# Optimization experiments

Measured on AMD Instinct MI355X. Metric: run time of the kernel, lower is better.

The kernel has to match this reference:

```python
import jax, jax.numpy as jnp
import numpy as np

NUM_RBF = 16; TOP_K = 32; EDGE_F = 128; NODE_F = 128; NUM_POS = 16; MAX_REL = 32
B, L, M = 2, 1024, 25
# atom order: N=0, Ca=1, C=2, O=3, Cb=4; 24 pairs after the (Ca,Ca) D_neighbors term,
# in the exact order of the torch forward's RBF_all list
PAIR_A = jnp.array([0,2,3,4,1,1,1,1,0,0,0,4,4,3,0,2,3,4,2,3,4,2,3,2])
PAIR_B = jnp.array([0,2,3,4,0,2,3,4,2,3,4,2,3,2,1,1,1,1,0,0,0,4,4,3])


def _rbf(D):
    mu = jnp.linspace(2.0, 22.0, NUM_RBF)
    sig = (22.0 - 2.0) / NUM_RBF
    return jnp.exp(-((D[..., None] - mu) / sig) ** 2)


def _ln(x, g, b, eps=1e-5):
    m = x.mean(-1, keepdims=True)
    v = ((x - m) ** 2).mean(-1, keepdims=True)
    return (x - m) * jax.lax.rsqrt(v + eps) * g + b


def _normalize(v):
    n = jnp.linalg.norm(v, axis=-1, keepdims=True)
    return v / jnp.maximum(n, 1e-12)


def setup_inputs():
    key = jax.random.key(0)
    ks = jax.random.split(key, 16)
    def w(i, shape, scale):
        return jax.random.normal(ks[i], shape, jnp.float32) * scale
    ar = jnp.arange(120, dtype=jnp.int32)
    return {
        "X": w(0, (B, L, 4, 3), 3.0),
        "Y": w(1, (B, L, M, 3), 3.0),
        "Y_m": jnp.ones((B, L, M), jnp.float32),
        "Y_t": jax.random.randint(ks[2], (B, L, M), 0, 120, jnp.int32),
        "mask": jnp.ones((B, L), jnp.float32),
        "R_idx": jnp.tile(jnp.arange(L, dtype=jnp.int32), (B, 1)),
        "chain_labels": jnp.zeros((B, L), jnp.int32),
        # learned params; torch Linear y = x @ W.T + b stored here as [in,out]
        "pos_W": w(3, (2 * MAX_REL + 2, NUM_POS), 0.1),
        "pos_b": jnp.zeros((NUM_POS,), jnp.float32),
        "edge_W": w(4, (NUM_POS + 25 * NUM_RBF, EDGE_F), 0.05),
        "ln_e_g": jnp.ones((EDGE_F,), jnp.float32), "ln_e_b": jnp.zeros((EDGE_F,), jnp.float32),
        "npd_W": w(5, (5 * NUM_RBF + 64 + 4, NODE_F), 0.08),
        "npd_b": jnp.zeros((NODE_F,), jnp.float32),
        "ln_n_g": jnp.ones((NODE_F,), jnp.float32), "ln_n_b": jnp.zeros((NODE_F,), jnp.float32),
        "type_W": w(6, (147, 64), 0.08), "type_b": jnp.zeros((64,), jnp.float32),
        "yn_W": w(7, (147, NODE_F), 0.08),
        "ye_W": w(8, (NUM_RBF, NODE_F), 0.2),
        "ln_ye_g": jnp.ones((NODE_F,), jnp.float32), "ln_ye_b": jnp.zeros((NODE_F,), jnp.float32),
        "ln_yn_g": jnp.ones((NODE_F,), jnp.float32), "ln_yn_b": jnp.zeros((NODE_F,), jnp.float32),
        # periodic table: [atomic_number, group(<19), period(<8)] per element id
        "ptable": jnp.stack([ar, ar % 19, ar % 8]),
    }


def reference(X, Y, Y_m, Y_t, mask, R_idx, chain_labels, pos_W, pos_b, edge_W,
              ln_e_g, ln_e_b, npd_W, npd_b, ln_n_g, ln_n_b, type_W, type_b,
              yn_W, ye_W, ln_ye_g, ln_ye_b, ln_yn_g, ln_yn_b, ptable):
    N, Ca, C, O = X[:, :, 0], X[:, :, 1], X[:, :, 2], X[:, :, 3]
    b = Ca - N; c = C - Ca
    a = jnp.cross(b, c)
    Cb = -0.58273431 * a + 0.56802827 * b - 0.54067466 * c + Ca

    # masked Ca-Ca distances + kNN (smallest)
    m2 = mask[:, :, None] * mask[:, None, :]
    D = m2 * jnp.sqrt(((Ca[:, :, None, :] - Ca[:, None, :, :]) ** 2).sum(-1) + 1e-6)
    D_adjust = D + (1.0 - m2) * D.max(-1, keepdims=True)
    k = min(TOP_K, L)
    neg_D, E_idx = jax.lax.top_k(-D_adjust, k)
    D_neighbors = -neg_D  # [B,L,k]

    atoms = jnp.stack([N, Ca, C, O, Cb])  # [5,B,L,3]
    def pair_rbf(ai, bi):
        A = atoms[ai]; Bc = atoms[bi]
        Dab = jnp.sqrt(((A[:, :, None, :] - Bc[:, None, :, :]) ** 2).sum(-1) + 1e-6)
        return _rbf(jnp.take_along_axis(Dab, E_idx, axis=2))  # [B,L,k,16]
    rbf_pairs = jax.vmap(pair_rbf)(PAIR_A, PAIR_B)  # [24,B,L,k,16]
    RBF_all = jnp.concatenate([_rbf(D_neighbors)[:, :, :, None, :],
                               jnp.moveaxis(rbf_pairs, 0, 3)], axis=3)
    RBF_all = RBF_all.reshape(RBF_all.shape[0], RBF_all.shape[1], k, 25 * NUM_RBF)

    # positional encodings over gathered neighbor offsets
    offset = jnp.take_along_axis(R_idx[:, :, None] - R_idx[:, None, :], E_idx, axis=2)
    d_chains = (chain_labels[:, :, None] == chain_labels[:, None, :]).astype(jnp.int32)
    E_chains = jnp.take_along_axis(d_chains, E_idx, axis=2)
    d = jnp.clip(offset + MAX_REL, 0, 2 * MAX_REL) * E_chains + (1 - E_chains) * (2 * MAX_REL + 1)
    E_pos = jax.nn.one_hot(d, 2 * MAX_REL + 2, dtype=jnp.float32) @ pos_W + pos_b

    E = jnp.concatenate([E_pos, RBF_all], -1) @ edge_W
    E = _ln(E, ln_e_g, ln_e_b)

    # ligand atom type features
    Y_t_1hot_ = jnp.concatenate([
        jax.nn.one_hot(Y_t, 120, dtype=jnp.float32),
        jax.nn.one_hot(ptable[1][Y_t], 19, dtype=jnp.float32),
        jax.nn.one_hot(ptable[2][Y_t], 8, dtype=jnp.float32)], -1)  # [B,L,M,147]
    Y_t_1hot = Y_t_1hot_ @ type_W + type_b  # [B,L,M,64]

    def rbf_to_Y(A):
        return _rbf(jnp.sqrt(((A[:, :, None, :] - Y) ** 2).sum(-1) + 1e-6))
    D_Y = jnp.concatenate([rbf_to_Y(A) for A in (N, Ca, C, O, Cb)], -1)  # [B,L,M,80]

    # local-frame angle features (A=N, B=Ca, C=C)
    e1 = _normalize(N - Ca)
    v2 = C - Ca
    e2 = _normalize(v2 - e1 * (e1 * v2).sum(-1, keepdims=True))
    e3 = jnp.cross(e1, e2)
    R_res = jnp.stack([e1, e2, e3], axis=-1)  # [B,L,3,3], columns e1,e2,e3
    local = jnp.einsum('blqp,blyq->blyp', R_res, Y - Ca[:, :, None, :])
    rxy = jnp.sqrt(local[..., 0] ** 2 + local[..., 1] ** 2 + 1e-8)
    rxyz = jnp.linalg.norm(local, axis=-1) + 1e-8
    f_angles = jnp.stack([local[..., 0] / rxy, local[..., 1] / rxy,
                          rxy / rxyz, local[..., 2] / rxyz], -1)  # [B,L,M,4]

    V = jnp.concatenate([D_Y, Y_t_1hot, f_angles], -1) @ npd_W + npd_b
    V = _ln(V, ln_n_g, ln_n_b)

    Y_edges = _rbf(jnp.sqrt(((Y[:, :, :, None, :] - Y[:, :, None, :, :]) ** 2).sum(-1) + 1e-6)) @ ye_W
    Y_edges = _ln(Y_edges, ln_ye_g, ln_ye_b)
    Y_nodes = _ln(Y_t_1hot_ @ yn_W, ln_yn_g, ln_yn_b)
    return V, E, E_idx, Y_nodes, Y_edges, Y_m
```

## Files before the change

kernel.cpp:

```cpp
#include <hip/hip_runtime.h>
#include <hip/hip_bf16.h>
#include <stdint.h>

#define BB 2
#define LLEN 1024
#define MM 25
#define KK 32

#define OFF_V   0
#define OFF_E   6553600
#define OFF_EI  14942208
#define OFF_YN  15007744
#define OFF_YE  21561344
#define OFF_YM  185401344

#define KD 416
#define KP 424
#define KP2 168
#define NR 5

#define SCRATCH_BYTES (680*1024)

typedef __attribute__((ext_vector_type(8))) short short8_t;
typedef __attribute__((ext_vector_type(4))) float f32x4;

__constant__ int g_PA[24] = {0,2,3,4,1,1,1,1,0,0,0,4,4,3,0,2,3,4,2,3,4,2,3,2};
__constant__ int g_PB[24] = {0,2,3,4,0,2,3,4,2,3,4,2,3,2,1,1,1,1,0,0,0,4,4,3};

__device__ __forceinline__ float rbf_val(float d, int r) {
    float mu = 2.0f + (20.0f / 15.0f) * (float)r;
    float z = (d - mu) * 0.8f;
    return __expf(-z * z);
}

__global__ __launch_bounds__(256) void k_pretopk(
    const float* __restrict__ X, const float* __restrict__ mask,
    const float* __restrict__ W, const float* __restrict__ yeW,
    const float* __restrict__ npdW,
    __hip_bfloat16* __restrict__ Bp, __hip_bfloat16* __restrict__ Bp2,
    __hip_bfloat16* __restrict__ Bp3,
    int* __restrict__ eidx, float* __restrict__ dnb,
    float* __restrict__ outEI)
{
    __shared__ float sx[1024], syy[1024], sz[1024], sm[1024];
    int tid = threadIdx.x;

    if (blockIdx.x >= 512) {
        int idx = (blockIdx.x - 512) * 256 + tid;
        if (idx < 6656) {
            int lane = idx & 63, tt = (idx >> 6) & 7, ks = idx >> 9;
            int k0 = ks*32 + (lane >> 4)*8;
            int n  = tt*16 + (lane & 15);
            __hip_bfloat16* dst = Bp + (size_t)idx * 8;
            #pragma unroll
            for (int j = 0; j < 8; ++j) dst[j] = __float2bfloat16(W[(size_t)(k0 + j)*128 + n]);
        } else if (idx < 7168) {
            int i2 = idx - 6656;
            int lane = i2 & 63, tt = i2 >> 6;
            int kg = lane >> 4;
            int n  = tt*16 + (lane & 15);
            __hip_bfloat16* dst = Bp2 + (size_t)i2 * 8;
            #pragma unroll
            for (int j = 0; j < 8; ++j) {
                float v = (kg < 2) ? yeW[(size_t)(kg*8 + j)*128 + n] : 0.0f;
                dst[j] = __float2bfloat16(v);
            }
        } else if (idx < 9728) {
            int i3 = idx - 7168;
            int lane = i3 & 63, tt = (i3 >> 6) & 7, ks = i3 >> 9;
            int k0 = ks*32 + (lane >> 4)*8;
            int n  = tt*16 + (lane & 15);
            __hip_bfloat16* dst = Bp3 + (size_t)i3 * 8;
            #pragma unroll
            for (int j = 0; j < 8; ++j) {
                int k = k0 + j;
                float v = (k < 148) ? npdW[(size_t)k*128 + n] : 0.0f;
                dst[j] = __float2bfloat16(v);
            }
        }
        return;
    }

    int wid = tid >> 6, lane = tid & 63;
    int row0 = blockIdx.x * 4;
    int b = row0 >> 10;
    const float* Xb = X + (size_t)b * LLEN * 12;
    const float* mb = mask + b * LLEN;
    for (int j = tid; j < 1024; j += 256) {
        sx[j]  = Xb[j*12+3];
        syy[j] = Xb[j*12+4];
        sz[j]  = Xb[j*12+5];
        sm[j]  = mb[j];
    }
    __syncthreads();

    int row = row0 + wid, i = row & 1023;
    float cax = sx[i], cay = syy[i], caz = sz[i];
    float mi = sm[i];

    float df[16], mm_[16];
    float lmax = 0.0f;
    #pragma unroll
    for (int q = 0; q < 16; ++q) {
        int j = q*64 + lane;
        float dx = cax - sx[j];
        float dy = cay - syy[j];
        float dz = caz - sz[j];
        float m2 = mi * sm[j];
        float d = sqrtf(dx*dx + dy*dy + dz*dz + 1e-6f) * m2;
        df[q] = d; mm_[q] = m2;
        lmax = fmaxf(lmax, d);
    }
    #pragma unroll
    for (int o = 32; o > 0; o >>= 1) lmax = fmaxf(lmax, __shfl_xor(lmax, o));

    unsigned long long pack[16];
    #pragma unroll
    for (int q = 0; q < 16; ++q) {
        float da = df[q] + (1.0f - mm_[q]) * lmax;
        pack[q] = ((unsigned long long)__float_as_uint(da) << 32) | (unsigned)(q*64 + lane);
    }

    int   myJw = 0;
    float myDv = 0.0f;
    for (int it = 0; it < KK; ++it) {
        unsigned long long lmin = pack[0];
        #pragma unroll
        for (int q = 1; q < 16; ++q) if (pack[q] < lmin) lmin = pack[q];
        #pragma unroll
        for (int o = 32; o > 0; o >>= 1) {
            unsigned long long other = __shfl_xor(lmin, o);
            if (other < lmin) lmin = other;
        }
        int jw = (int)(lmin & 0xffffffffu);
        if (lane == it) { myJw = jw; myDv = __uint_as_float((unsigned)(lmin >> 32)); }
        int lw = jw & 63, qw = jw >> 6;
        #pragma unroll
        for (int q = 0; q < 16; ++q)
            if (lane == lw && q == qw) pack[q] = ~0ull;
    }
    if (lane < KK) {
        eidx[row*KK + lane]  = myJw;
        dnb [row*KK + lane]  = myDv;
        outEI[row*KK + lane] = (float)myJw;
    }
}

__global__ __launch_bounds__(256) void k_edges(
    const float* __restrict__ X,
    const int* __restrict__ Ridx, const int* __restrict__ chain,
    const float* __restrict__ posW, const float* __restrict__ posb,
    const __hip_bfloat16* __restrict__ Bpack,
    const float* __restrict__ lnEg, const float* __restrict__ lnEb,
    const int* __restrict__ eidx, const float* __restrict__ dnb,
    float* __restrict__ outE)
{
    __shared__ __align__(16) __hip_bfloat16 A[64 * KP];
    __shared__ float aj[64][16];
    __shared__ float ai[2][16];
    __shared__ int   didx[64];
    int r0 = blockIdx.x * 2;
    int b  = r0 >> 10;
    int tid = threadIdx.x;
    const float* Xb = X + (size_t)b * LLEN * 12;

    if (tid < 64) {
        int e = tid, row = r0 + (e >> 5), k = e & 31;
        int j = eidx[row*KK + k];
        const float* xr = Xb + j*12;
        float nx=xr[0], ny=xr[1], nz=xr[2];
        float ax=xr[3], ay=xr[4], az=xr[5];
        float cx=xr[6], cy=xr[7], cz=xr[8];
        float bx=ax-nx, by=ay-ny, bz=az-nz;
        float vx=cx-ax, vy=cy-ay, vz=cz-az;
        float qx = by*vz - bz*vy, qy = bz*vx - bx*vz, qz = bx*vy - by*vx;
        aj[e][0]=nx; aj[e][1]=ny; aj[e][2]=nz;
        aj[e][3]=ax; aj[e][4]=ay; aj[e][5]=az;
        aj[e][6]=cx; aj[e][7]=cy; aj[e][8]=cz;
        aj[e][9]=xr[9]; aj[e][10]=xr[10]; aj[e][11]=xr[11];
        aj[e][12] = -0.58273431f*qx + 0.56802827f*bx - 0.54067466f*vx + ax;
        aj[e][13] = -0.58273431f*qy + 0.56802827f*by - 0.54067466f*vy + ay;
        aj[e][14] = -0.58273431f*qz + 0.56802827f*bz - 0.54067466f*vz + az;
        int off = Ridx[row] - Ridx[b*LLEN + j];
        int ec = (chain[row] == chain[b*LLEN + j]) ? 1 : 0;
        int dc = off + 32; dc = dc < 0 ? 0 : (dc > 64 ? 64 : dc);
        didx[e] = ec ? dc : 65;
    }
    if (tid >= 64 && tid < 66) {
        int rl = tid - 64;
        int i = (r0 + rl) & 1023;
        const float* xr = Xb + i*12;
        float nx=xr[0], ny=xr[1], nz=xr[2];
        float ax=xr[3], ay=xr[4], az=xr[5];
        float cx=xr[6], cy=xr[7], cz=xr[8];
        float bx=ax-nx, by=ay-ny, bz=az-nz;
        float vx=cx-ax, vy=cy-ay, vz=cz-az;
        float qx = by*vz - bz*vy, qy = bz*vx - bx*vz, qz = bx*vy - by*vx;
        ai[rl][0]=nx; ai[rl][1]=ny; ai[rl][2]=nz;
        ai[rl][3]=ax; ai[rl][4]=ay; ai[rl][5]=az;
        ai[rl][6]=cx; ai[rl][7]=cy; ai[rl][8]=cz;
        ai[rl][9]=xr[9]; ai[rl][10]=xr[10]; ai[rl][11]=xr[11];
        ai[rl][12] = -0.58273431f*qx + 0.56802827f*bx - 0.54067466f*vx + ax;
        ai[rl][13] = -0.58273431f*qy + 0.56802827f*by - 0.54067466f*vy + ay;
        ai[rl][14] = -0.58273431f*qz + 0.56802827f*bz - 0.54067466f*vz + az;
    }
    __syncthreads();

    for (int item = tid; item < 64 * 26; item += 256) {
        int e = item / 26, it = item - e * 26;
        int rl = e >> 5;
        union { short8_t v[2]; __hip_bfloat16 h[16]; } uf;
        if (it == 0) {
            int d = didx[e];
            #pragma unroll
            for (int c = 0; c < 16; ++c) uf.h[c] = __float2bfloat16(posW[d*16 + c] + posb[c]);
        } else {
            float dist;
            if (it == 1) {
                dist = dnb[(r0 + rl)*KK + (e & 31)];
            } else {
                int p = it - 2;
                int a = g_PA[p], q = g_PB[p];
                float dx = ai[rl][a*3+0] - aj[e][q*3+0];
                float dy = ai[rl][a*3+1] - aj[e][q*3+1];
                float dz = ai[rl][a*3+2] - aj[e][q*3+2];
                dist = sqrtf(dx*dx + dy*dy + dz*dz + 1e-6f);
            }
            #pragma unroll
            for (int r = 0; r < 16; ++r) uf.h[r] = __float2bfloat16(rbf_val(dist, r));
        }
        short8_t* dst = (short8_t*)(A + e * KP + it * 16);
        dst[0] = uf.v[0];
        dst[1] = uf.v[1];
    }
    __syncthreads();

    int wid = tid >> 6, lane = tid & 63;
    int col16 = lane & 15, kg = lane >> 4;
    f32x4 acc[8];
    #pragma unroll
    for (int t = 0; t < 8; ++t) acc[t] = (f32x4){0.f, 0.f, 0.f, 0.f};
    const __hip_bfloat16* Ar = A + (wid*16 + col16) * KP + kg * 8;
    const short8_t* Bp = (const short8_t*)Bpack;
    for (int ks = 0; ks < 13; ++ks) {
        short8_t a = *(const short8_t*)(Ar + ks*32);
        #pragma unroll
        for (int t = 0; t < 8; ++t) {
            short8_t bf = Bp[(ks*8 + t)*64 + lane];
            acc[t] = __builtin_amdgcn_mfma_f32_16x16x32_bf16(a, bf, acc[t], 0, 0, 0);
        }
    }
    __syncthreads();

    float* sbuf = (float*)A + wid * (16*132);
    float g[8], be[8];
    #pragma unroll
    for (int t = 0; t < 8; ++t) { g[t] = lnEg[t*16 + col16]; be[t] = lnEb[t*16 + col16]; }
    #pragma unroll
    for (int r = 0; r < 4; ++r) {
        float s = 0.0f;
        #pragma unroll
        for (int t = 0; t < 8; ++t) s += acc[t][r];
        s += __shfl_xor(s, 1); s += __shfl_xor(s, 2);
        s += __shfl_xor(s, 4); s += __shfl_xor(s, 8);
        float mean = s * (1.0f/128.0f);
        float q2 = 0.0f;
        #pragma unroll
        for (int t = 0; t < 8; ++t) { float c0 = acc[t][r] - mean; q2 += c0*c0; }
        q2 += __shfl_xor(q2, 1); q2 += __shfl_xor(q2, 2);
        q2 += __shfl_xor(q2, 4); q2 += __shfl_xor(q2, 8);
        float inv = rsqrtf(q2 * (1.0f/128.0f) + 1e-5f);
        float* sr = sbuf + (kg*4 + r) * 132;
        #pragma unroll
        for (int t = 0; t < 8; ++t) sr[t*16 + col16] = (acc[t][r] - mean)*inv*g[t] + be[t];
    }
    float* gdst = outE + ((size_t)r0 * KK + wid*16) * 128;
    #pragma unroll
    for (int it = 0; it < 8; ++it) {
        int off = it*256 + lane*4;
        int rr = off >> 7, cc = off & 127;
        float4 v = *(const float4*)(sbuf + rr*132 + cc);
        *(float4*)(gdst + off) = v;
    }
}

__global__ __launch_bounds__(256) void k_nodes(
    const float* __restrict__ X, const float* __restrict__ Y,
    const int* __restrict__ Yt,
    const float* __restrict__ typeW, const float* __restrict__ typeb,
    const int* __restrict__ ptab,
    const __hip_bfloat16* __restrict__ Bpack3, const float* __restrict__ npdb,
    const float* __restrict__ lnNg, const float* __restrict__ lnNb,
    float* __restrict__ outV)
{
    __shared__ __align__(16) __hip_bfloat16 A[128 * KP2];
    __shared__ float sat[NR][15];
    __shared__ float sfr[NR][9];
    int r0 = blockIdx.x * NR;
    int nrows = (2048 - r0) < NR ? (2048 - r0) : NR;
    int natoms = nrows * MM;
    int tid = threadIdx.x;

    if (tid < nrows) {
        int row = r0 + tid;
        int b = row >> 10, i = row & 1023;
        const float* xr = X + ((size_t)b * LLEN + i) * 12;
        float nx=xr[0], ny=xr[1], nz=xr[2];
        float ax=xr[3], ay=xr[4], az=xr[5];
        float cx=xr[6], cy=xr[7], cz=xr[8];
        float bx=ax-nx, by=ay-ny, bz=az-nz;
        float vx=cx-ax, vy=cy-ay, vz=cz-az;
        float qx = by*vz - bz*vy, qy = bz*vx - bx*vz, qz = bx*vy - by*vx;
        sat[tid][0]=nx; sat[tid][1]=ny; sat[tid][2]=nz;
        sat[tid][3]=ax; sat[tid][4]=ay; sat[tid][5]=az;
        sat[tid][6]=cx; sat[tid][7]=cy; sat[tid][8]=cz;
        sat[tid][9]=xr[9]; sat[tid][10]=xr[10]; sat[tid][11]=xr[11];
        sat[tid][12] = -0.58273431f*qx + 0.56802827f*bx - 0.54067466f*vx + ax;
        sat[tid][13] = -0.58273431f*qy + 0.56802827f*by - 0.54067466f*vy + ay;
        sat[tid][14] = -0.58273431f*qz + 0.56802827f*bz - 0.54067466f*vz + az;
        float e1x = nx-ax, e1y = ny-ay, e1z = nz-az;
        float n1 = fmaxf(sqrtf(e1x*e1x+e1y*e1y+e1z*e1z), 1e-12f);
        e1x/=n1; e1y/=n1; e1z/=n1;
        float dd = e1x*vx + e1y*vy + e1z*vz;
        float u2x = vx - e1x*dd, u2y = vy - e1y*dd, u2z = vz - e1z*dd;
        float n2 = fmaxf(sqrtf(u2x*u2x+u2y*u2y+u2z*u2z), 1e-12f);
        u2x/=n2; u2y/=n2; u2z/=n2;
        sfr[tid][0]=e1x; sfr[tid][1]=e1y; sfr[tid][2]=e1z;
        sfr[tid][3]=u2x; sfr[tid][4]=u2y; sfr[tid][5]=u2z;
        sfr[tid][6]=e1y*u2z - e1z*u2y;
        sfr[tid][7]=e1z*u2x - e1x*u2z;
        sfr[tid][8]=e1x*u2y - e1y*u2x;
    }
    __syncthreads();

    for (int item = tid; item < natoms * 10; item += 256) {
        int a = item / 10, it = item - a * 10;
        int rl = a / MM, m = a - rl * MM;
        int row = r0 + rl;
        const float* Yb = Y + (size_t)row * MM * 3 + m * 3;
        union { short8_t v[2]; __hip_bfloat16 h[16]; } uf;
        if (it < 5) {
            float dx = sat[rl][it*3+0] - Yb[0];
            float dy = sat[rl][it*3+1] - Yb[1];
            float dz = sat[rl][it*3+2] - Yb[2];
            float dist = sqrtf(dx*dx + dy*dy + dz*dz + 1e-6f);
            #pragma unroll
            for (int r = 0; r < 16; ++r) uf.h[r] = __float2bfloat16(rbf_val(dist, r));
        } else if (it < 9) {
            int qq = it - 5;
            int t = Yt[row*MM + m];
            int p1 = ptab[120 + t], p2 = ptab[240 + t];
            #pragma unroll
            for (int c = 0; c < 16; ++c) {
                int cc = qq*16 + c;
                uf.h[c] = __float2bfloat16(typeW[t*64 + cc] + typeW[(120+p1)*64 + cc]
                        + typeW[(139+p2)*64 + cc] + typeb[cc]);
            }
        } else {
            float vx = Yb[0] - sat[rl][3];
            float vy = Yb[1] - sat[rl][4];
            float vz = Yb[2] - sat[rl][5];
            float l0 = sfr[rl][0]*vx + sfr[rl][1]*vy + sfr[rl][2]*vz;
            float l1 = sfr[rl][3]*vx + sfr[rl][4]*vy + sfr[rl][5]*vz;
            float l2 = sfr[rl][6]*vx + sfr[rl][7]*vy + sfr[rl][8]*vz;
            float rxy  = sqrtf(l0*l0 + l1*l1 + 1e-8f);
            float rxyz = sqrtf(l0*l0 + l1*l1 + l2*l2) + 1e-8f;
            uf.h[0] = __float2bfloat16(l0 / rxy);
            uf.h[1] = __float2bfloat16(l1 / rxy);
            uf.h[2] = __float2bfloat16(rxy / rxyz);
            uf.h[3] = __float2bfloat16(l2 / rxyz);
            #pragma unroll
            for (int c = 4; c < 16; ++c) uf.h[c] = __float2bfloat16(0.0f);
        }
        short8_t* dst = (short8_t*)(A + a * KP2 + it * 16);
        dst[0] = uf.v[0];
        dst[1] = uf.v[1];
    }
    __syncthreads();

    int wid = tid >> 6, lane = tid & 63;
    int col16 = lane & 15, kg = lane >> 4;
    const short8_t* Bp = (const short8_t*)Bpack3;
    float g[8], be[8], bias[8];
    #pragma unroll
    for (int t = 0; t < 8; ++t) {
        g[t] = lnNg[t*16 + col16]; be[t] = lnNb[t*16 + col16];
        bias[t] = npdb[t*16 + col16];
    }
    #pragma unroll
    for (int half = 0; half < 2; ++half) {
        int tile = wid + half*4;
        int abase = tile * 16;
        if (abase < natoms) {
            const __hip_bfloat16* Ar = A + (abase + col16) * KP2 + kg * 8;
            f32x4 acc[8];
            #pragma unroll
            for (int t = 0; t < 8; ++t) acc[t] = (f32x4){0.f, 0.f, 0.f, 0.f};
            for (int ks = 0; ks < 5; ++ks) {
                short8_t a = *(const short8_t*)(Ar + ks*32);
                #pragma unroll
                for (int t = 0; t < 8; ++t) {
                    short8_t bf = Bp[(ks*8 + t)*64 + lane];
                    acc[t] = __builtin_amdgcn_mfma_f32_16x16x32_bf16(a, bf, acc[t], 0, 0, 0);
                }
            }
            #pragma unroll
            for (int r = 0; r < 4; ++r) {
                float s = 0.0f;
                #pragma unroll
                for (int t = 0; t < 8; ++t) { acc[t][r] += bias[t]; s += acc[t][r]; }
                s += __shfl_xor(s, 1); s += __shfl_xor(s, 2);
                s += __shfl_xor(s, 4); s += __shfl_xor(s, 8);
                float mean = s * (1.0f/128.0f);
                float q2 = 0.0f;
                #pragma unroll
                for (int t = 0; t < 8; ++t) { float c0 = acc[t][r] - mean; q2 += c0*c0; }
                q2 += __shfl_xor(q2, 1); q2 += __shfl_xor(q2, 2);
                q2 += __shfl_xor(q2, 4); q2 += __shfl_xor(q2, 8);
                float inv = rsqrtf(q2 * (1.0f/128.0f) + 1e-5f);
                int aa = abase + kg*4 + r;
                if (aa < natoms) {
                    float* dst = outV + ((size_t)r0 * MM + aa) * 128 + col16;
                    #pragma unroll
                    for (int t = 0; t < 8; ++t) dst[t*16] = (acc[t][r] - mean)*inv*g[t] + be[t];
                }
            }
        }
    }
}

__global__ __launch_bounds__(256) void k_ymerge(
    int block_base,
    const float* __restrict__ Y,
    const __hip_bfloat16* __restrict__ Bpack2,
    const float* __restrict__ lnYEg, const float* __restrict__ lnYEb,
    float* __restrict__ outYE,
    const int* __restrict__ Yt, const float* __restrict__ Ym,
    const int* __restrict__ ptab, const float* __restrict__ ynW,
    const float* __restrict__ lnYNg, const float* __restrict__ lnYNb,
    float* __restrict__ outYN, float* __restrict__ outYM)
{
    __shared__ __align__(16) float sy4[32][4];
    __shared__ __align__(16) float stage[4][16*132];
    int vbid = blockIdx.x + block_base;
    int tid = threadIdx.x;
    int wv = tid >> 6, lane = tid & 63;

    if (vbid >= BB*LLEN) {
        int row = (vbid - BB*LLEN) * 4 + wv;
        int t = Yt[row];
        int p1 = ptab[120 + t], p2 = ptab[240 + t];
        int r0 = t, r1 = 120 + p1, r2 = 139 + p2;
        float x0 = ynW[r0*128 + lane] + ynW[r1*128 + lane] + ynW[r2*128 + lane];
        float x1 = ynW[r0*128 + 64 + lane] + ynW[r1*128 + 64 + lane] + ynW[r2*128 + 64 + lane];
        float s = x0 + x1, s2 = x0*x0 + x1*x1;
        #pragma unroll
        for (int o = 1; o < 64; o <<= 1) { s += __shfl_xor(s, o); s2 += __shfl_xor(s2, o); }
        float mean = s * (1.0f/128.0f);
        float var  = s2 * (1.0f/128.0f) - mean*mean;
        float inv  = rsqrtf(var + 1e-5f);
        size_t base = (size_t)row * 128;
        outYN[base + lane]      = (x0 - mean)*inv*lnYNg[lane]    + lnYNb[lane];
        outYN[base + 64 + lane] = (x1 - mean)*inv*lnYNg[64+lane] + lnYNb[64+lane];
        if (lane == 0) outYM[row] = Ym[row];
        return;
    }

    int row = vbid;
    int col16 = lane & 15, kg = lane >> 4;

    if (tid < 32) { sy4[tid][0]=0.f; sy4[tid][1]=0.f; sy4[tid][2]=0.f; sy4[tid][3]=0.f; }
    __syncthreads();
    if (tid < MM*3) ((float*)sy4)[ (tid/3)*4 + (tid%3) ] = Y[(size_t)row * MM * 3 + tid];

    short8_t bfr[8];
    const short8_t* B2 = (const short8_t*)Bpack2;
    #pragma unroll
    for (int t = 0; t < 8; ++t) bfr[t] = B2[t*64 + lane];
    float g[8], be[8];
    #pragma unroll
    for (int t = 0; t < 8; ++t) { g[t] = lnYEg[t*16 + col16]; be[t] = lnYEb[t*16 + col16]; }
    __syncthreads();

    float* outR = outYE + (size_t)row * 625 * 128;
    float* sbuf = stage[wv];
    for (int T = wv; T < 40; T += 4) {
        int p0 = T * 16;
        int p  = p0 + col16;
        int pc = p < 624 ? p : 624;
        int m1 = pc / 25, m2 = pc - 25*m1;
        float dx = sy4[m1][0] - sy4[m2][0];
        float dy = sy4[m1][1] - sy4[m2][1];
        float dz = sy4[m1][2] - sy4[m2][2];
        float d = sqrtf(dx*dx + dy*dy + dz*dz + 1e-6f);
        union { short8_t v; __hip_bfloat16 h[8]; } ua;
        if (kg < 2) {
            #pragma unroll
            for (int j = 0; j < 8; ++j) ua.h[j] = __float2bfloat16(rbf_val(d, kg*8 + j));
        } else {
            ua.v = (short8_t){0,0,0,0,0,0,0,0};
        }
        f32x4 acc[8];
        #pragma unroll
        for (int t = 0; t < 8; ++t)
            acc[t] = __builtin_amdgcn_mfma_f32_16x16x32_bf16(ua.v, bfr[t],
                         (f32x4){0.f,0.f,0.f,0.f}, 0, 0, 0);
        #pragma unroll
        for (int r = 0; r < 4; ++r) {
            float s = 0.0f;
            #pragma unroll
            for (int t = 0; t < 8; ++t) s += acc[t][r];
            s += __shfl_xor(s, 1); s += __shfl_xor(s, 2);
            s += __shfl_xor(s, 4); s += __shfl_xor(s, 8);
            float mean = s * (1.0f/128.0f);
            float q2 = 0.0f;
            #pragma unroll
            for (int t = 0; t < 8; ++t) { float c0 = acc[t][r] - mean; q2 += c0*c0; }
            q2 += __shfl_xor(q2, 1); q2 += __shfl_xor(q2, 2);
            q2 += __shfl_xor(q2, 4); q2 += __shfl_xor(q2, 8);
            float inv = rsqrtf(q2 * (1.0f/128.0f) + 1e-5f);
            float* sr = sbuf + (kg*4 + r) * 132;
            #pragma unroll
            for (int t = 0; t < 8; ++t) sr[t*16 + col16] = (acc[t][r] - mean)*inv*g[t] + be[t];
        }
        #pragma unroll
        for (int it = 0; it < 8; ++it) {
            int off = it*256 + lane*4;
            int rr = (off >> 7), cc = off & 127;
            float4 v = *(const float4*)(sbuf + rr*132 + cc);
            int gbase = p0*128 + off;
            if (gbase < 80000) *(float4*)(outR + gbase) = v;
        }
    }
}

extern "C" void kernel_launch(void* const* d_in, const int* in_sizes, int n_in,
                              void* d_out, int out_size, void* d_ws, size_t ws_size,
                              hipStream_t stream) {
    const float* X     = (const float*)d_in[0];
    const float* Y     = (const float*)d_in[1];
    const float* Ym    = (const float*)d_in[2];
    const int*   Yt    = (const int*)d_in[3];
    const float* mask  = (const float*)d_in[4];
    const int*   Ridx  = (const int*)d_in[5];
    const int*   chain = (const int*)d_in[6];
    const float* posW  = (const float*)d_in[7];
    const float* posb  = (const float*)d_in[8];
    const float* edgeW = (const float*)d_in[9];
    const float* lnEg  = (const float*)d_in[10];
    const float* lnEb  = (const float*)d_in[11];
    const float* npdW  = (const float*)d_in[12];
    const float* npdb  = (const float*)d_in[13];
    const float* lnNg  = (const float*)d_in[14];
    const float* lnNb  = (const float*)d_in[15];
    const float* typeW = (const float*)d_in[16];
    const float* typeb = (const float*)d_in[17];
    const float* ynW   = (const float*)d_in[18];
    const float* yeW   = (const float*)d_in[19];
    const float* lnYEg = (const float*)d_in[20];
    const float* lnYEb = (const float*)d_in[21];
    const float* lnYNg = (const float*)d_in[22];
    const float* lnYNb = (const float*)d_in[23];
    const int*   ptab  = (const int*)d_in[24];

    float* o = (float*)d_out;
    bool ws_ok = (ws_size >= (size_t)SCRATCH_BYTES);
    char* scratch = ws_ok ? (char*)d_ws : (char*)(o + OFF_YN);
    int*   eidx = (int*)scratch;
    float* dnb  = (float*)(scratch + BB*LLEN*KK*4);
    __hip_bfloat16* Bpack  = (__hip_bfloat16*)(scratch + 2*BB*LLEN*KK*4);
    __hip_bfloat16* Bpack2 = Bpack + 6656*8;
    __hip_bfloat16* Bpack3 = Bpack2 + 512*8;

    k_pretopk<<<550, 256, 0, stream>>>(X, mask, edgeW, yeW, npdW,
                                       Bpack, Bpack2, Bpack3,
                                       eidx, dnb, o + OFF_EI);
    k_edges <<<BB*LLEN/2, 256, 0, stream>>>(X, Ridx, chain, posW, posb, Bpack,
                                            lnEg, lnEb, eidx, dnb, o + OFF_E);
    k_nodes <<<(BB*LLEN + NR - 1)/NR, 256, 0, stream>>>(X, Y, Yt, typeW, typeb, ptab,
                                          Bpack3, npdb, lnNg, lnNb, o + OFF_V);
    if (ws_ok) {
        k_ymerge<<<BB*LLEN + BB*LLEN*MM/4, 256, 0, stream>>>(0,
            Y, Bpack2, lnYEg, lnYEb, o + OFF_YE,
            Yt, Ym, ptab, ynW, lnYNg, lnYNb, o + OFF_YN, o + OFF_YM);
    } else {
        k_ymerge<<<BB*LLEN, 256, 0, stream>>>(0,
            Y, Bpack2, lnYEg, lnYEb, o + OFF_YE,
            Yt, Ym, ptab, ynW, lnYNg, lnYNb, o + OFF_YN, o + OFF_YM);
        k_ymerge<<<BB*LLEN*MM/4, 256, 0, stream>>>(BB*LLEN,
            Y, Bpack2, lnYEg, lnYEb, o + OFF_YE,
            Yt, Ym, ptab, ynW, lnYNg, lnYNb, o + OFF_YN, o + OFF_YM);
    }
}
```

Before: 241.8 us.

## Merge edge, node and Y-feature kernels into one launch with virtual block dispatch

Combines the k_edges, k_nodes and k_ymerge kernels into a single k_main kernel. Each block picks its role from a virtual block index, and the per-role shared-memory buffers are overlaid in a union. This removes two kernel launches and the serialization between them, so the small edge and node grids can run alongside the large Y-edge grid. The cost is that the union takes the largest shared-memory footprint and register pressure comes from the heaviest branch, which may reduce occupancy for the lighter roles.

Measured after the change: 239.8 us. No clear change (-0.8%).

```diff
diff --git a/kernel.cpp b/kernel.cpp
--- a/kernel.cpp
+++ b/kernel.cpp
@@ -14,10 +14,18 @@
 #define OFF_YE  21561344
 #define OFF_YM  185401344
 
-#define KD 416
 #define KP 424
 #define KP2 168
 #define NR 5
+
+#define NB_YE  (BB*LLEN)
+#define NB_E   (BB*LLEN/2)
+#define NB_N   ((BB*LLEN+NR-1)/NR)
+#define NB_YN  (BB*LLEN*MM/4)
+#define VB_E   NB_YE
+#define VB_N   (VB_E + NB_E)
+#define VB_YN  (VB_N + NB_N)
+#define VB_END (VB_YN + NB_YN)
 
 #define SCRATCH_BYTES (680*1024)
 
@@ -146,308 +154,41 @@
     }
 }
 
-__global__ __launch_bounds__(256) void k_edges(
-    const float* __restrict__ X,
+union SMem {
+    struct { __hip_bfloat16 A[64*KP]; float aj[64][16]; float ai[2][16]; int didx[64]; } e;
+    struct { __hip_bfloat16 A[128*KP2]; float sat[NR][15]; float sfr[NR][9]; } n;
+    struct { float sy4[32][4]; float stage[4][16*132]; } y;
+};
+
+__global__ __launch_bounds__(256) void k_main(
+    int vbase,
+    const float* __restrict__ X, const float* __restrict__ Y,
     const int* __restrict__ Ridx, const int* __restrict__ chain,
     const float* __restrict__ posW, const float* __restrict__ posb,
     const __hip_bfloat16* __restrict__ Bpack,
     const float* __restrict__ lnEg, const float* __restrict__ lnEb,
     const int* __restrict__ eidx, const float* __restrict__ dnb,
-    float* __restrict__ outE)
-{
-    __shared__ __align__(16) __hip_bfloat16 A[64 * KP];
-    __shared__ float aj[64][16];
-    __shared__ float ai[2][16];
-    __shared__ int   didx[64];
-    int r0 = blockIdx.x * 2;
-    int b  = r0 >> 10;
-    int tid = threadIdx.x;
-    const float* Xb = X + (size_t)b * LLEN * 12;
-
-    if (tid < 64) {
-        int e = tid, row = r0 + (e >> 5), k = e & 31;
-        int j = eidx[row*KK + k];
-        const float* xr = Xb + j*12;
-        float nx=xr[0], ny=xr[1], nz=xr[2];
-        float ax=xr[3], ay=xr[4], az=xr[5];
-        float cx=xr[6], cy=xr[7], cz=xr[8];
-        float bx=ax-nx, by=ay-ny, bz=az-nz;
-        float vx=cx-ax, vy=cy-ay, vz=cz-az;
-        float qx = by*vz - bz*vy, qy = bz*vx - bx*vz, qz = bx*vy - by*vx;
-        aj[e][0]=nx; aj[e][1]=ny; aj[e][2]=nz;
-        aj[e][3]=ax; aj[e][4]=ay; aj[e][5]=az;
-        aj[e][6]=cx; aj[e][7]=cy; aj[e][8]=cz;
-        aj[e][9]=xr[9]; aj[e][10]=xr[10]; aj[e][11]=xr[11];
-        aj[e][12] = -0.58273431f*qx + 0.56802827f*bx - 0.54067466f*vx + ax;
-        aj[e][13] = -0.58273431f*qy + 0.56802827f*by - 0.54067466f*vy + ay;
-        aj[e][14] = -0.58273431f*qz + 0.56802827f*bz - 0.54067466f*vz + az;
-        int off = Ridx[row] - Ridx[b*LLEN + j];
-        int ec = (chain[row] == chain[b*LLEN + j]) ? 1 : 0;
-        int dc = off + 32; dc = dc < 0 ? 0 : (dc > 64 ? 64 : dc);
-        didx[e] = ec ? dc : 65;
-    }
-    if (tid >= 64 && tid < 66) {
-        int rl = tid - 64;
-        int i = (r0 + rl) & 1023;
-        const float* xr = Xb + i*12;
-        float nx=xr[0], ny=xr[1], nz=xr[2];
-        float ax=xr[3], ay=xr[4], az=xr[5];
-        float cx=xr[6], cy=xr[7], cz=xr[8];
-        float bx=ax-nx, by=ay-ny, bz=az-nz;
-        float vx=cx-ax, vy=cy-ay, vz=cz-az;
-        float qx = by*vz - bz*vy, qy = bz*vx - bx*vz, qz = bx*vy - by*vx;
-        ai[rl][0]=nx; ai[rl][1]=ny; ai[rl][2]=nz;
-        ai[rl][3]=ax; ai[rl][4]=ay; ai[rl][5]=az;
-        ai[rl][6]=cx; ai[rl][7]=cy; ai[rl][8]=cz;
-        ai[rl][9]=xr[9]; ai[rl][10]=xr[10]; ai[rl][11]=xr[11];
-        ai[rl][12] = -0.58273431f*qx + 0.56802827f*bx - 0.54067466f*vx + ax;
-        ai[rl][13] = -0.58273431f*qy + 0.56802827f*by - 0.54067466f*vy + ay;
-        ai[rl][14] = -0.58273431f*qz + 0.56802827f*bz - 0.54067466f*vz + az;
-    }
-    __syncthreads();
-
-    for (int item = tid; item < 64 * 26; item += 256) {
-        int e = item / 26, it = item - e * 26;
-        int rl = e >> 5;
-        union { short8_t v[2]; __hip_bfloat16 h[16]; } uf;
-        if (it == 0) {
-            int d = didx[e];
-            #pragma unroll
-            for (int c = 0; c < 16; ++c) uf.h[c] = __float2bfloat16(posW[d*16 + c] + posb[c]);
-        } else {
-            float dist;
-            if (it == 1) {
-                dist = dnb[(r0 + rl)*KK + (e & 31)];
-            } else {
-                int p = it - 2;
-                int a = g_PA[p], q = g_PB[p];
-                float dx = ai[rl][a*3+0] - aj[e][q*3+0];
-                float dy = ai[rl][a*3+1] - aj[e][q*3+1];
-                float dz = ai[rl][a*3+2] - aj[e][q*3+2];
-                dist = sqrtf(dx*dx + dy*dy + dz*dz + 1e-6f);
-            }
-            #pragma unroll
-            for (int r = 0; r < 16; ++r) uf.h[r] = __float2bfloat16(rbf_val(dist, r));
-        }
-        short8_t* dst = (short8_t*)(A + e * KP + it * 16);
-        dst[0] = uf.v[0];
-        dst[1] = uf.v[1];
-    }
-    __syncthreads();
-
-    int wid = tid >> 6, lane = tid & 63;
-    int col16 = lane & 15, kg = lane >> 4;
-    f32x4 acc[8];
-    #pragma unroll
-    for (int t = 0; t < 8; ++t) acc[t] = (f32x4){0.f, 0.f, 0.f, 0.f};
-    const __hip_bfloat16* Ar = A + (wid*16 + col16) * KP + kg * 8;
-    const short8_t* Bp = (const short8_t*)Bpack;
-    for (int ks = 0; ks < 13; ++ks) {
-        short8_t a = *(const short8_t*)(Ar + ks*32);
-        #pragma unroll
-        for (int t = 0; t < 8; ++t) {
-            short8_t bf = Bp[(ks*8 + t)*64 + lane];
-            acc[t] = __builtin_amdgcn_mfma_f32_16x16x32_bf16(a, bf, acc[t], 0, 0, 0);
-        }
-    }
-    __syncthreads();
-
-    float* sbuf = (float*)A + wid * (16*132);
-    float g[8], be[8];
-    #pragma unroll
-    for (int t = 0; t < 8; ++t) { g[t] = lnEg[t*16 + col16]; be[t] = lnEb[t*16 + col16]; }
-    #pragma unroll
-    for (int r = 0; r < 4; ++r) {
-        float s = 0.0f;
-        #pragma unroll
-        for (int t = 0; t < 8; ++t) s += acc[t][r];
-        s += __shfl_xor(s, 1); s += __shfl_xor(s, 2);
-        s += __shfl_xor(s, 4); s += __shfl_xor(s, 8);
-        float mean = s * (1.0f/128.0f);
-        float q2 = 0.0f;
-        #pragma unroll
-        for (int t = 0; t < 8; ++t) { float c0 = acc[t][r] - mean; q2 += c0*c0; }
-        q2 += __shfl_xor(q2, 1); q2 += __shfl_xor(q2, 2);
-        q2 += __shfl_xor(q2, 4); q2 += __shfl_xor(q2, 8);
-        float inv = rsqrtf(q2 * (1.0f/128.0f) + 1e-5f);
-        float* sr = sbuf + (kg*4 + r) * 132;
-        #pragma unroll
-        for (int t = 0; t < 8; ++t) sr[t*16 + col16] = (acc[t][r] - mean)*inv*g[t] + be[t];
-    }
-    float* gdst = outE + ((size_t)r0 * KK + wid*16) * 128;
-    #pragma unroll
-    for (int it = 0; it < 8; ++it) {
-        int off = it*256 + lane*4;
-        int rr = off >> 7, cc = off & 127;
-        float4 v = *(const float4*)(sbuf + rr*132 + cc);
-        *(float4*)(gdst + off) = v;
-    }
-}
-
-__global__ __launch_bounds__(256) void k_nodes(
-    const float* __restrict__ X, const float* __restrict__ Y,
     const int* __restrict__ Yt,
     const float* __restrict__ typeW, const float* __restrict__ typeb,
     const int* __restrict__ ptab,
     const __hip_bfloat16* __restrict__ Bpack3, const float* __restrict__ npdb,
     const float* __restrict__ lnNg, const float* __restrict__ lnNb,
-    float* __restrict__ outV)
-{
-    __shared__ __align__(16) __hip_bfloat16 A[128 * KP2];
-    __shared__ float sat[NR][15];
-    __shared__ float sfr[NR][9];
-    int r0 = blockIdx.x * NR;
-    int nrows = (2048 - r0) < NR ? (2048 - r0) : NR;
-    int natoms = nrows * MM;
-    int tid = threadIdx.x;
-
-    if (tid < nrows) {
-        int row = r0 + tid;
-        int b = row >> 10, i = row & 1023;
-        const float* xr = X + ((size_t)b * LLEN + i) * 12;
-        float nx=xr[0], ny=xr[1], nz=xr[2];
-        float ax=xr[3], ay=xr[4], az=xr[5];
-        float cx=xr[6], cy=xr[7], cz=xr[8];
-        float bx=ax-nx, by=ay-ny, bz=az-nz;
-        float vx=cx-ax, vy=cy-ay, vz=cz-az;
-        float qx = by*vz - bz*vy, qy = bz*vx - bx*vz, qz = bx*vy - by*vx;
-        sat[tid][0]=nx; sat[tid][1]=ny; sat[tid][2]=nz;
-        sat[tid][3]=ax; sat[tid][4]=ay; sat[tid][5]=az;
-        sat[tid][6]=cx; sat[tid][7]=cy; sat[tid][8]=cz;
-        sat[tid][9]=xr[9]; sat[tid][10]=xr[10]; sat[tid][11]=xr[11];
-        sat[tid][12] = -0.58273431f*qx + 0.56802827f*bx - 0.54067466f*vx + ax;
-        sat[tid][13] = -0.58273431f*qy + 0.56802827f*by - 0.54067466f*vy + ay;
-        sat[tid][14] = -0.58273431f*qz + 0.56802827f*bz - 0.54067466f*vz + az;
-        float e1x = nx-ax, e1y = ny-ay, e1z = nz-az;
-        float n1 = fmaxf(sqrtf(e1x*e1x+e1y*e1y+e1z*e1z), 1e-12f);
-        e1x/=n1; e1y/=n1; e1z/=n1;
-        float dd = e1x*vx + e1y*vy + e1z*vz;
-        float u2x = vx - e1x*dd, u2y = vy - e1y*dd, u2z = vz - e1z*dd;
-        float n2 = fmaxf(sqrtf(u2x*u2x+u2y*u2y+u2z*u2z), 1e-12f);
-        u2x/=n2; u2y/=n2; u2z/=n2;
-        sfr[tid][0]=e1x; sfr[tid][1]=e1y; sfr[tid][2]=e1z;
-        sfr[tid][3]=u2x; sfr[tid][4]=u2y; sfr[tid][5]=u2z;
-        sfr[tid][6]=e1y*u2z - e1z*u2y;
-        sfr[tid][7]=e1z*u2x - e1x*u2z;
-        sfr[tid][8]=e1x*u2y - e1y*u2x;
-    }
-    __syncthreads();
-
-    for (int item = tid; item < natoms * 10; item += 256) {
-        int a = item / 10, it = item - a * 10;
-        int rl = a / MM, m = a - rl * MM;
-        int row = r0 + rl;
-        const float* Yb = Y + (size_t)row * MM * 3 + m * 3;
-        union { short8_t v[2]; __hip_bfloat16 h[16]; } uf;
-        if (it < 5) {
-            float dx = sat[rl][it*3+0] - Yb[0];
-            float dy = sat[rl][it*3+1] - Yb[1];
-            float dz = sat[rl][it*3+2] - Yb[2];
-            float dist = sqrtf(dx*dx + dy*dy + dz*dz + 1e-6f);
-            #pragma unroll
-            for (int r = 0; r < 16; ++r) uf.h[r] = __float2bfloat16(rbf_val(dist, r));
-        } else if (it < 9) {
-            int qq = it - 5;
-            int t = Yt[row*MM + m];
-            int p1 = ptab[120 + t], p2 = ptab[240 + t];
-            #pragma unroll
-            for (int c = 0; c < 16; ++c) {
-                int cc = qq*16 + c;
-                uf.h[c] = __float2bfloat16(typeW[t*64 + cc] + typeW[(120+p1)*64 + cc]
-                        + typeW[(139+p2)*64 + cc] + typeb[cc]);
-            }
-        } else {
-            float vx = Yb[0] - sat[rl][3];
-            float vy = Yb[1] - sat[rl][4];
-            float vz = Yb[2] - sat[rl][5];
-            float l0 = sfr[rl][0]*vx + sfr[rl][1]*vy + sfr[rl][2]*vz;
-            float l1 = sfr[rl][3]*vx + sfr[rl][4]*vy + sfr[rl][5]*vz;
-            float l2 = sfr[rl][6]*vx + sfr[rl][7]*vy + sfr[rl][8]*vz;
-            float rxy  = sqrtf(l0*l0 + l1*l1 + 1e-8f);
-            float rxyz = sqrtf(l0*l0 + l1*l1 + l2*l2) + 1e-8f;
-            uf.h[0] = __float2bfloat16(l0 / rxy);
-            uf.h[1] = __float2bfloat16(l1 / rxy);
-            uf.h[2] = __float2bfloat16(rxy / rxyz);
-            uf.h[3] = __float2bfloat16(l2 / rxyz);
-            #pragma unroll
-            for (int c = 4; c < 16; ++c) uf.h[c] = __float2bfloat16(0.0f);
-        }
-        short8_t* dst = (short8_t*)(A + a * KP2 + it * 16);
-        dst[0] = uf.v[0];
-        dst[1] = uf.v[1];
-    }
-    __syncthreads();
-
-    int wid = tid >> 6, lane = tid & 63;
-    int col16 = lane & 15, kg = lane >> 4;
-    const short8_t* Bp = (const short8_t*)Bpack3;
-    float g[8], be[8], bias[8];
-    #pragma unroll
-    for (int t = 0; t < 8; ++t) {
-        g[t] = lnNg[t*16 + col16]; be[t] = lnNb[t*16 + col16];
-        bias[t] = npdb[t*16 + col16];
-    }
-    #pragma unroll
-    for (int half = 0; half < 2; ++half) {
-        int tile = wid + half*4;
-        int abase = tile * 16;
-        if (abase < natoms) {
-            const __hip_bfloat16* Ar = A + (abase + col16) * KP2 + kg * 8;
-            f32x4 acc[8];
-            #pragma unroll
-            for (int t = 0; t < 8; ++t) acc[t] = (f32x4){0.f, 0.f, 0.f, 0.f};
-            for (int ks = 0; ks < 5; ++ks) {
-                short8_t a = *(const short8_t*)(Ar + ks*32);
-                #pragma unroll
-                for (int t = 0; t < 8; ++t) {
-                    short8_t bf = Bp[(ks*8 + t)*64 + lane];
-                    acc[t] = __builtin_amdgcn_mfma_f32_16x16x32_bf16(a, bf, acc[t], 0, 0, 0);
-                }
-            }
-            #pragma unroll
-            for (int r = 0; r < 4; ++r) {
-                float s = 0.0f;
-                #pragma unroll
-                for (int t = 0; t < 8; ++t) { acc[t][r] += bias[t]; s += acc[t][r]; }
-                s += __shfl_xor(s, 1); s += __shfl_xor(s, 2);
-                s += __shfl_xor(s, 4); s += __shfl_xor(s, 8);
-                float mean = s * (1.0f/128.0f);
-                float q2 = 0.0f;
-                #pragma unroll
-                for (int t = 0; t < 8; ++t) { float c0 = acc[t][r] - mean; q2 += c0*c0; }
-                q2 += __shfl_xor(q2, 1); q2 += __shfl_xor(q2, 2);
-                q2 += __shfl_xor(q2, 4); q2 += __shfl_xor(q2, 8);
-                float inv = rsqrtf(q2 * (1.0f/128.0f) + 1e-5f);
-                int aa = abase + kg*4 + r;
-                if (aa < natoms) {
-                    float* dst = outV + ((size_t)r0 * MM + aa) * 128 + col16;
-                    #pragma unroll
-                    for (int t = 0; t < 8; ++t) dst[t*16] = (acc[t][r] - mean)*inv*g[t] + be[t];
-                }
-            }
-        }
-    }
-}
-
-__global__ __launch_bounds__(256) void k_ymerge(
-    int block_base,
-    const float* __restrict__ Y,
     const __hip_bfloat16* __restrict__ Bpack2,
     const float* __restrict__ lnYEg, const float* __restrict__ lnYEb,
-    float* __restrict__ outYE,
-    const int* __restrict__ Yt, const float* __restrict__ Ym,
-    const int* __restrict__ ptab, const float* __restrict__ ynW,
+    const float* __restrict__ Ym, const float* __restrict__ ynW,
     const float* __restrict__ lnYNg, const float* __restrict__ lnYNb,
-    float* __restrict__ outYN, float* __restrict__ outYM)
+    float* __restrict__ outV, float* __restrict__ outE,
+    float* __restrict__ outYN, float* __restrict__ outYE,
+    float* __restrict__ outYM)
 {
-    __shared__ __align__(16) float sy4[32][4];
-    __shared__ __align__(16) float stage[4][16*132];
-    int vbid = blockIdx.x + block_base;
+    __shared__ __align__(16) SMem sm;
+    int vb = blockIdx.x + vbase;
     int tid = threadIdx.x;
     int wv = tid >> 6, lane = tid & 63;
-
-    if (vbid >= BB*LLEN) {
-        int row = (vbid - BB*LLEN) * 4 + wv;
+    int col16 = lane & 15, kg = lane >> 4;
+
+    if (vb >= VB_YN) {
+        int row = (vb - VB_YN) * 4 + wv;
         int t = Yt[row];
         int p1 = ptab[120 + t], p2 = ptab[240 + t];
         int r0 = t, r1 = 120 + p1, r2 = 139 + p2;
@@ -466,45 +207,170 @@
         return;
     }
 
-    int row = vbid;
-    int col16 = lane & 15, kg = lane >> 4;
-
-    if (tid < 32) { sy4[tid][0]=0.f; sy4[tid][1]=0.f; sy4[tid][2]=0.f; sy4[tid][3]=0.f; }
-    __syncthreads();
-    if (tid < MM*3) ((float*)sy4)[ (tid/3)*4 + (tid%3) ] = Y[(size_t)row * MM * 3 + tid];
-
-    short8_t bfr[8];
-    const short8_t* B2 = (const short8_t*)Bpack2;
-    #pragma unroll
-    for (int t = 0; t < 8; ++t) bfr[t] = B2[t*64 + lane];
-    float g[8], be[8];
-    #pragma unroll
-    for (int t = 0; t < 8; ++t) { g[t] = lnYEg[t*16 + col16]; be[t] = lnYEb[t*16 + col16]; }
-    __syncthreads();
-
-    float* outR = outYE + (size_t)row * 625 * 128;
-    float* sbuf = stage[wv];
-    for (int T = wv; T < 40; T += 4) {
-        int p0 = T * 16;
-        int p  = p0 + col16;
-        int pc = p < 624 ? p : 624;
-        int m1 = pc / 25, m2 = pc - 25*m1;
-        float dx = sy4[m1][0] - sy4[m2][0];
-        float dy = sy4[m1][1] - sy4[m2][1];
-        float dz = sy4[m1][2] - sy4[m2][2];
-        float d = sqrtf(dx*dx + dy*dy + dz*dz + 1e-6f);
-        union { short8_t v; __hip_bfloat16 h[8]; } ua;
-        if (kg < 2) {
-            #pragma unroll
-            for (int j = 0; j < 8; ++j) ua.h[j] = __float2bfloat16(rbf_val(d, kg*8 + j));
-        } else {
-            ua.v = (short8_t){0,0,0,0,0,0,0,0};
-        }
+    if (vb < NB_YE) {
+        int row = vb;
+        if (tid < 32) { sm.y.sy4[tid][0]=0.f; sm.y.sy4[tid][1]=0.f; sm.y.sy4[tid][2]=0.f; sm.y.sy4[tid][3]=0.f; }
+        __syncthreads();
+        if (tid < MM*3) ((float*)sm.y.sy4)[ (tid/3)*4 + (tid%3) ] = Y[(size_t)row * MM * 3 + tid];
+
+        short8_t bfr[8];
+        const short8_t* B2 = (const short8_t*)Bpack2;
+        #pragma unroll
+        for (int t = 0; t < 8; ++t) bfr[t] = B2[t*64 + lane];
+        float g[8], be[8];
+        #pragma unroll
+        for (int t = 0; t < 8; ++t) { g[t] = lnYEg[t*16 + col16]; be[t] = lnYEb[t*16 + col16]; }
+        __syncthreads();
+
+        float* outR = outYE + (size_t)row * 625 * 128;
+        float* sbuf = sm.y.stage[wv];
+        for (int T = wv; T < 40; T += 4) {
+            int p0 = T * 16;
+            int p  = p0 + col16;
+            int pc = p < 624 ? p : 624;
+            int m1 = pc / 25, m2 = pc - 25*m1;
+            float dx = sm.y.sy4[m1][0] - sm.y.sy4[m2][0];
+            float dy = sm.y.sy4[m1][1] - sm.y.sy4[m2][1];
+            float dz = sm.y.sy4[m1][2] - sm.y.sy4[m2][2];
+            float d = sqrtf(dx*dx + dy*dy + dz*dz + 1e-6f);
+            union { short8_t v; __hip_bfloat16 h[8]; } ua;
+            if (kg < 2) {
+                #pragma unroll
+                for (int j = 0; j < 8; ++j) ua.h[j] = __float2bfloat16(rbf_val(d, kg*8 + j));
+            } else {
+                ua.v = (short8_t){0,0,0,0,0,0,0,0};
+            }
+            f32x4 acc[8];
+            #pragma unroll
+            for (int t = 0; t < 8; ++t)
+                acc[t] = __builtin_amdgcn_mfma_f32_16x16x32_bf16(ua.v, bfr[t],
+                             (f32x4){0.f,0.f,0.f,0.f}, 0, 0, 0);
+            #pragma unroll
+            for (int r = 0; r < 4; ++r) {
+                float s = 0.0f;
+                #pragma unroll
+                for (int t = 0; t < 8; ++t) s += acc[t][r];
+                s += __shfl_xor(s, 1); s += __shfl_xor(s, 2);
+                s += __shfl_xor(s, 4); s += __shfl_xor(s, 8);
+                float mean = s * (1.0f/128.0f);
+                float q2 = 0.0f;
+                #pragma unroll
+                for (int t = 0; t < 8; ++t) { float c0 = acc[t][r] - mean; q2 += c0*c0; }
+                q2 += __shfl_xor(q2, 1); q2 += __shfl_xor(q2, 2);
+                q2 += __shfl_xor(q2, 4); q2 += __shfl_xor(q2, 8);
+                float inv = rsqrtf(q2 * (1.0f/128.0f) + 1e-5f);
+                float* sr = sbuf + (kg*4 + r) * 132;
+                #pragma unroll
+                for (int t = 0; t < 8; ++t) sr[t*16 + col16] = (acc[t][r] - mean)*inv*g[t] + be[t];
+            }
+            #pragma unroll
+            for (int it = 0; it < 8; ++it) {
+                int off = it*256 + lane*4;
+                int rr = (off >> 7), cc = off & 127;
+                float4 v = *(const float4*)(sbuf + rr*132 + cc);
+                int gbase = p0*128 + off;
+                if (gbase < 80000) *(float4*)(outR + gbase) = v;
+            }
+        }
+        return;
+    }
+
+    if (vb < VB_N) {
+        int r0 = (vb - VB_E) * 2;
+        int b  = r0 >> 10;
+        const float* Xb = X + (size_t)b * LLEN * 12;
+
+        if (tid < 64) {
+            int e = tid, row = r0 + (e >> 5), k = e & 31;
+            int j = eidx[row*KK + k];
+            const float* xr = Xb + j*12;
+            float nx=xr[0], ny=xr[1], nz=xr[2];
+            float ax=xr[3], ay=xr[4], az=xr[5];
+            float cx=xr[6], cy=xr[7], cz=xr[8];
+            float bx=ax-nx, by=ay-ny, bz=az-nz;
+            float vx=cx-ax, vy=cy-ay, vz=cz-az;
+            float qx = by*vz - bz*vy, qy = bz*vx - bx*vz, qz = bx*vy - by*vx;
+            sm.e.aj[e][0]=nx; sm.e.aj[e][1]=ny; sm.e.aj[e][2]=nz;
+            sm.e.aj[e][3]=ax; sm.e.aj[e][4]=ay; sm.e.aj[e][5]=az;
+            sm.e.aj[e][6]=cx; sm.e.aj[e][7]=cy; sm.e.aj[e][8]=cz;
+            sm.e.aj[e][9]=xr[9]; sm.e.aj[e][10]=xr[10]; sm.e.aj[e][11]=xr[11];
+            sm.e.aj[e][12] = -0.58273431f*qx + 0.56802827f*bx - 0.54067466f*vx + ax;
+            sm.e.aj[e][13] = -0.58273431f*qy + 0.56802827f*by - 0.54067466f*vy + ay;
+            sm.e.aj[e][14] = -0.58273431f*qz + 0.56802827f*bz - 0.54067466f*vz + az;
+            int off = Ridx[row] - Ridx[b*LLEN + j];
+            int ec = (chain[row] == chain[b*LLEN + j]) ? 1 : 0;
+            int dc = off + 32; dc = dc < 0 ? 0 : (dc > 64 ? 64 : dc);
+            sm.e.didx[e] = ec ? dc : 65;
+        }
+        if (tid >= 64 && tid < 66) {
+            int rl = tid - 64;
+            int i = (r0 + rl) & 1023;
+            const float* xr = Xb + i*12;
+            float nx=xr[0], ny=xr[1], nz=xr[2];
+            float ax=xr[3], ay=xr[4], az=xr[5];
+            float cx=xr[6], cy=xr[7], cz=xr[8];
+            float bx=ax-nx, by=ay-ny, bz=az-nz;
+            float vx=cx-ax, vy=cy-ay, vz=cz-az;
+            float qx = by*vz - bz*vy, qy = bz*vx - bx*vz, qz = bx*vy - by*vx;
+            sm.e.ai[rl][0]=nx; sm.e.ai[rl][1]=ny; sm.e.ai[rl][2]=nz;
+            sm.e.ai[rl][3]=ax; sm.e.ai[rl][4]=ay; sm.e.ai[rl][5]=az;
+            sm.e.ai[rl][6]=cx; sm.e.ai[rl][7]=cy; sm.e.ai[rl][8]=cz;
+            sm.e.ai[rl][9]=xr[9]; sm.e.ai[rl][10]=xr[10]; sm.e.ai[rl][11]=xr[11];
+            sm.e.ai[rl][12] = -0.58273431f*qx + 0.56802827f*bx - 0.54067466f*vx + ax;
+            sm.e.ai[rl][13] = -0.58273431f*qy + 0.56802827f*by - 0.54067466f*vy + ay;
+            sm.e.ai[rl][14] = -0.58273431f*qz + 0.56802827f*bz - 0.54067466f*vz + az;
+        }
+        __syncthreads();
+
+        for (int item = tid; item < 64 * 26; item += 256) {
+            int e = item / 26, it = item - e * 26;
+            int rl = e >> 5;
+            union { short8_t v[2]; __hip_bfloat16 h[16]; } uf;
+            if (it == 0) {
+                int d = sm.e.didx[e];
+                #pragma unroll
+                for (int c = 0; c < 16; ++c) uf.h[c] = __float2bfloat16(posW[d*16 + c] + posb[c]);
+            } else {
+                float dist;
+                if (it == 1) {
+                    dist = dnb[(r0 + rl)*KK + (e & 31)];
+                } else {
+                    int p = it - 2;
+                    int a = g_PA[p], q = g_PB[p];
+                    float dx = sm.e.ai[rl][a*3+0] - sm.e.aj[e][q*3+0];
+                    float dy = sm.e.ai[rl][a*3+1] - sm.e.aj[e][q*3+1];
+                    float dz = sm.e.ai[rl][a*3+2] - sm.e.aj[e][q*3+2];
+                    dist = sqrtf(dx*dx + dy*dy + dz*dz + 1e-6f);
+                }
+                #pragma unroll
+                for (int r = 0; r < 16; ++r) uf.h[r] = __float2bfloat16(rbf_val(dist, r));
+            }
+            short8_t* dst = (short8_t*)(sm.e.A + e * KP + it * 16);
+            dst[0] = uf.v[0];
+            dst[1] = uf.v[1];
+        }
+        __syncthreads();
+
+        int wid = tid >> 6;
         f32x4 acc[8];
         #pragma unroll
-        for (int t = 0; t < 8; ++t)
-            acc[t] = __builtin_amdgcn_mfma_f32_16x16x32_bf16(ua.v, bfr[t],
-                         (f32x4){0.f,0.f,0.f,0.f}, 0, 0, 0);
+        for (int t = 0; t < 8; ++t) acc[t] = (f32x4){0.f, 0.f, 0.f, 0.f};
+        const __hip_bfloat16* Ar = sm.e.A + (wid*16 + col16) * KP + kg * 8;
+        const short8_t* Bp = (const short8_t*)Bpack;
+        for (int ks = 0; ks < 13; ++ks) {
+            short8_t a = *(const short8_t*)(Ar + ks*32);
+            #pragma unroll
+            for (int t = 0; t < 8; ++t) {
+                short8_t bf = Bp[(ks*8 + t)*64 + lane];
+                acc[t] = __builtin_amdgcn_mfma_f32_16x16x32_bf16(a, bf, acc[t], 0, 0, 0);
+            }
+        }
+        __syncthreads();
+
+        float* sbuf = (float*)sm.e.A + wid * (16*132);
+        float g[8], be[8];
+        #pragma unroll
+        for (int t = 0; t < 8; ++t) { g[t] = lnEg[t*16 + col16]; be[t] = lnEb[t*16 + col16]; }
         #pragma unroll
         for (int r = 0; r < 4; ++r) {
             float s = 0.0f;
@@ -523,13 +389,146 @@
             #pragma unroll
             for (int t = 0; t < 8; ++t) sr[t*16 + col16] = (acc[t][r] - mean)*inv*g[t] + be[t];
         }
+        float* gdst = outE + ((size_t)r0 * KK + wid*16) * 128;
         #pragma unroll
         for (int it = 0; it < 8; ++it) {
             int off = it*256 + lane*4;
-            int rr = (off >> 7), cc = off & 127;
+            int rr = off >> 7, cc = off & 127;
             float4 v = *(const float4*)(sbuf + rr*132 + cc);
-            int gbase = p0*128 + off;
-            if (gbase < 80000) *(float4*)(outR + gbase) = v;
+            *(float4*)(gdst + off) = v;
+        }
+        return;
+    }
+
+    {
+        int r0 = (vb - VB_N) * NR;
+        int nrows = (2048 - r0) < NR ? (2048 - r0) : NR;
+        int natoms = nrows * MM;
+
+        if (tid < nrows) {
+            int row = r0 + tid;
+            int b = row >> 10, i = row & 1023;
+            const float* xr = X + ((size_t)b * LLEN + i) * 12;
+            float nx=xr[0], ny=xr[1], nz=xr[2];
+            float ax=xr[3], ay=xr[4], az=xr[5];
+            float cx=xr[6], cy=xr[7], cz=xr[8];
+            float bx=ax-nx, by=ay-ny, bz=az-nz;
+            float vx=cx-ax, vy=cy-ay, vz=cz-az;
+            float qx = by*vz - bz*vy, qy = bz*vx - bx*vz, qz = bx*vy - by*vx;
+            sm.n.sat[tid][0]=nx; sm.n.sat[tid][1]=ny; sm.n.sat[tid][2]=nz;
+            sm.n.sat[tid][3]=ax; sm.n.sat[tid][4]=ay; sm.n.sat[tid][5]=az;
+            sm.n.sat[tid][6]=cx; sm.n.sat[tid][7]=cy; sm.n.sat[tid][8]=cz;
+            sm.n.sat[tid][9]=xr[9]; sm.n.sat[tid][10]=xr[10]; sm.n.sat[tid][11]=xr[11];
+            sm.n.sat[tid][12] = -0.58273431f*qx + 0.56802827f*bx - 0.54067466f*vx + ax;
+            sm.n.sat[tid][13] = -0.58273431f*qy + 0.56802827f*by - 0.54067466f*vy + ay;
+            sm.n.sat[tid][14] = -0.58273431f*qz + 0.56802827f*bz - 0.54067466f*vz + az;
+            float e1x = nx-ax, e1y = ny-ay, e1z = nz-az;
+            float n1 = fmaxf(sqrtf(e1x*e1x+e1y*e1y+e1z*e1z), 1e-12f);
+            e1x/=n1; e1y/=n1; e1z/=n1;
+            float dd = e1x*vx + e1y*vy + e1z*vz;
+            float u2x = vx - e1x*dd, u2y = vy - e1y*dd, u2z = vz - e1z*dd;
+            float n2 = fmaxf(sqrtf(u2x*u2x+u2y*u2y+u2z*u2z), 1e-12f);
+            u2x/=n2; u2y/=n2; u2z/=n2;
+            sm.n.sfr[tid][0]=e1x; sm.n.sfr[tid][1]=e1y; sm.n.sfr[tid][2]=e1z;
+            sm.n.sfr[tid][3]=u2x; sm.n.sfr[tid][4]=u2y; sm.n.sfr[tid][5]=u2z;
+            sm.n.sfr[tid][6]=e1y*u2z - e1z*u2y;
+            sm.n.sfr[tid][7]=e1z*u2x - e1x*u2z;
+            sm.n.sfr[tid][8]=e1x*u2y - e1y*u2x;
+        }
+        __syncthreads();
+
+        for (int item = tid; item < natoms * 10; item += 256) {
+            int a = item / 10, it = item - a * 10;
+            int rl = a / MM, m = a - rl * MM;
+            int row = r0 + rl;
+            const float* Yb = Y + (size_t)row * MM * 3 + m * 3;
+            union { short8_t v[2]; __hip_bfloat16 h[16]; } uf;
+            if (it < 5) {
+                float dx = sm.n.sat[rl][it*3+0] - Yb[0];
+                float dy = sm.n.sat[rl][it*3+1] - Yb[1];
+                float dz = sm.n.sat[rl][it*3+2] - Yb[2];
+                float dist = sqrtf(dx*dx + dy*dy + dz*dz + 1e-6f);
+                #pragma unroll
+                for (int r = 0; r < 16; ++r) uf.h[r] = __float2bfloat16(rbf_val(dist, r));
+            } else if (it < 9) {
+                int qq = it - 5;
+                int t = Yt[row*MM + m];
+                int p1 = ptab[120 + t], p2 = ptab[240 + t];
+                #pragma unroll
+                for (int c = 0; c < 16; ++c) {
+                    int cc = qq*16 + c;
+                    uf.h[c] = __float2bfloat16(typeW[t*64 + cc] + typeW[(120+p1)*64 + cc]
+                            + typeW[(139+p2)*64 + cc] + typeb[cc]);
+                }
+            } else {
+                float vx = Yb[0] - sm.n.sat[rl][3];
+                float vy = Yb[1] - sm.n.sat[rl][4];
+                float vz = Yb[2] - sm.n.sat[rl][5];
+                float l0 = sm.n.sfr[rl][0]*vx + sm.n.sfr[rl][1]*vy + sm.n.sfr[rl][2]*vz;
+                float l1 = sm.n.sfr[rl][3]*vx + sm.n.sfr[rl][4]*vy + sm.n.sfr[rl][5]*vz;
+                float l2 = sm.n.sfr[rl][6]*vx + sm.n.sfr[rl][7]*vy + sm.n.sfr[rl][8]*vz;
+                float rxy  = sqrtf(l0*l0 + l1*l1 + 1e-8f);
+                float rxyz = sqrtf(l0*l0 + l1*l1 + l2*l2) + 1e-8f;
+                uf.h[0] = __float2bfloat16(l0 / rxy);
+                uf.h[1] = __float2bfloat16(l1 / rxy);
+                uf.h[2] = __float2bfloat16(rxy / rxyz);
+                uf.h[3] = __float2bfloat16(l2 / rxyz);
+                #pragma unroll
+                for (int c = 4; c < 16; ++c) uf.h[c] = __float2bfloat16(0.0f);
+            }
+            short8_t* dst = (short8_t*)(sm.n.A + a * KP2 + it * 16);
+            dst[0] = uf.v[0];
+            dst[1] = uf.v[1];
+        }
+        __syncthreads();
+
+        int wid = tid >> 6;
+        const short8_t* Bp = (const short8_t*)Bpack3;
+        float g[8], be[8], bias[8];
+        #pragma unroll
+        for (int t = 0; t < 8; ++t) {
+            g[t] = lnNg[t*16 + col16]; be[t] = lnNb[t*16 + col16];
+            bias[t] = npdb[t*16 + col16];
+        }
+        #pragma unroll
+        for (int half = 0; half < 2; ++half) {
+            int tile = wid + half*4;
+            int abase = tile * 16;
+            if (abase < natoms) {
+                const __hip_bfloat16* Ar = sm.n.A + (abase + col16) * KP2 + kg * 8;
+                f32x4 acc[8];
+                #pragma unroll
+                for (int t = 0; t < 8; ++t) acc[t] = (f32x4){0.f, 0.f, 0.f, 0.f};
+                for (int ks = 0; ks < 5; ++ks) {
+                    short8_t a = *(const short8_t*)(Ar + ks*32);
+                    #pragma unroll
+                    for (int t = 0; t < 8; ++t) {
+                        short8_t bf = Bp[(ks*8 + t)*64 + lane];
+                        acc[t] = __builtin_amdgcn_mfma_f32_16x16x32_bf16(a, bf, acc[t], 0, 0, 0);
+                    }
+                }
+                #pragma unroll
+                for (int r = 0; r < 4; ++r) {
+                    float s = 0.0f;
+                    #pragma unroll
+                    for (int t = 0; t < 8; ++t) { acc[t][r] += bias[t]; s += acc[t][r]; }
+                    s += __shfl_xor(s, 1); s += __shfl_xor(s, 2);
+                    s += __shfl_xor(s, 4); s += __shfl_xor(s, 8);
+                    float mean = s * (1.0f/128.0f);
+                    float q2 = 0.0f;
+                    #pragma unroll
+                    for (int t = 0; t < 8; ++t) { float c0 = acc[t][r] - mean; q2 += c0*c0; }
+                    q2 += __shfl_xor(q2, 1); q2 += __shfl_xor(q2, 2);
+                    q2 += __shfl_xor(q2, 4); q2 += __shfl_xor(q2, 8);
+                    float inv = rsqrtf(q2 * (1.0f/128.0f) + 1e-5f);
+                    int aa = abase + kg*4 + r;
+                    if (aa < natoms) {
+                        float* dst = outV + ((size_t)r0 * MM + aa) * 128 + col16;
+                        #pragma unroll
+                        for (int t = 0; t < 8; ++t) dst[t*16] = (acc[t][r] - mean)*inv*g[t] + be[t];
+                    }
+                }
+            }
         }
     }
 }
@@ -575,20 +574,22 @@
     k_pretopk<<<550, 256, 0, stream>>>(X, mask, edgeW, yeW, npdW,
                                        Bpack, Bpack2, Bpack3,
                                        eidx, dnb, o + OFF_EI);
-    k_edges <<<BB*LLEN/2, 256, 0, stream>>>(X, Ridx, chain, posW, posb, Bpack,
-                                            lnEg, lnEb, eidx, dnb, o + OFF_E);
-    k_nodes <<<(BB*LLEN + NR - 1)/NR, 256, 0, stream>>>(X, Y, Yt, typeW, typeb, ptab,
-                                          Bpack3, npdb, lnNg, lnNb, o + OFF_V);
     if (ws_ok) {
-        k_ymerge<<<BB*LLEN + BB*LLEN*MM/4, 256, 0, stream>>>(0,
-            Y, Bpack2, lnYEg, lnYEb, o + OFF_YE,
-            Yt, Ym, ptab, ynW, lnYNg, lnYNb, o + OFF_YN, o + OFF_YM);
+        k_main<<<VB_END, 256, 0, stream>>>(0,
+            X, Y, Ridx, chain, posW, posb, Bpack, lnEg, lnEb, eidx, dnb,
+            Yt, typeW, typeb, ptab, Bpack3, npdb, lnNg, lnNb,
+            Bpack2, lnYEg, lnYEb, Ym, ynW, lnYNg, lnYNb,
+            o + OFF_V, o + OFF_E, o + OFF_YN, o + OFF_YE, o + OFF_YM);
     } else {
-        k_ymerge<<<BB*LLEN, 256, 0, stream>>>(0,
-            Y, Bpack2, lnYEg, lnYEb, o + OFF_YE,
-            Yt, Ym, ptab, ynW, lnYNg, lnYNb, o + OFF_YN, o + OFF_YM);
-        k_ymerge<<<BB*LLEN*MM/4, 256, 0, stream>>>(BB*LLEN,
-            Y, Bpack2, lnYEg, lnYEb, o + OFF_YE,
-            Yt, Ym, ptab, ynW, lnYNg, lnYNb, o + OFF_YN, o + OFF_YM);
+        k_main<<<VB_YN, 256, 0, stream>>>(0,
+            X, Y, Ridx, chain, posW, posb, Bpack, lnEg, lnEb, eidx, dnb,
+            Yt, typeW, typeb, ptab, Bpack3, npdb, lnNg, lnNb,
+            Bpack2, lnYEg, lnYEb, Ym, ynW, lnYNg, lnYNb,
+            o + OFF_V, o + OFF_E, o + OFF_YN, o + OFF_YE, o + OFF_YM);
+        k_main<<<NB_YN, 256, 0, stream>>>(VB_YN,
+            X, Y, Ridx, chain, posW, posb, Bpack, lnEg, lnEb, eidx, dnb,
+            Yt, typeW, typeb, ptab, Bpack3, npdb, lnNg, lnNb,
+            Bpack2, lnYEg, lnYEb, Ym, ynW, lnYNg, lnYNb,
+            o + OFF_V, o + OFF_E, o + OFF_YN, o + OFF_YE, o + OFF_YM);
     }
 }
```
